# Kernel optimization log

Measured on AMD Instinct MI355X. Metric: run time of the kernel, lower is better.

Reference implementation:

```python
import jax, jax.numpy as jnp
import numpy as np

N_HEADS = 8
HEAD_DIM = 64  # d_model // n_heads = 512 // 8


def setup_inputs() -> dict:
    key = jax.random.key(0)
    kq, kk, kv, km = jax.random.split(key, 4)
    B, C, H, L, D = 8, 4, N_HEADS, 512, HEAD_DIM
    q = jax.random.normal(kq, (B * C, H, L, D), dtype=jnp.float32)
    k = jax.random.normal(kk, (B * C, H, D, L), dtype=jnp.float32)  # pre-transposed, matmul(q, k) directly
    v = jax.random.normal(kv, (B * C, H, L, D), dtype=jnp.float32)
    attn_mask = jax.random.randint(km, (B, L, L), 0, 2).astype(bool)  # True = masked out
    return {"q": q, "k": k, "v": v, "attn_mask": attn_mask}


def reference(q, k, v, attn_mask):
    # q: [B*C, H, L, D]; k: [B*C, H, D, L]; v: [B*C, H, L, D]; attn_mask: [B, L, L] bool
    scale = jnp.asarray(HEAD_DIM ** (-0.5), dtype=q.dtype)
    scores = jnp.einsum('ghld,ghdm->ghlm', q, k) * scale  # [B*C, H, L, L]
    if attn_mask is not None:
        B = attn_mask.shape[0]
        C = q.shape[0] // B
        H, L = scores.shape[1], scores.shape[2]
        scores = scores.reshape(B, C, H, L, L)
        mask = attn_mask[:, None, None, :, :]  # broadcast over channels and heads
        scores = jnp.where(mask, -jnp.inf, scores)
        scores = scores.reshape(B * C, H, L, L)
    attn_weights = jax.nn.softmax(scores, axis=-1)  # dropout p=0.0 -> identity (eval)
    output = jnp.einsum('ghlm,ghmd->ghld', attn_weights, v)  # [B*C, H, L, D]
    return output
```

## Files before the change

### kernel.cpp

```cpp
#include <hip/hip_runtime.h>


typedef __attribute__((ext_vector_type(8)))  short bf16x8;
typedef __attribute__((ext_vector_type(16))) float f32x16;

union Frag4 { uint4 x; unsigned u[4]; bf16x8 v; };

__device__ __forceinline__ unsigned pk_bf16(float a, float b){
    unsigned ua = __builtin_bit_cast(unsigned, a) + 0x8000u;
    unsigned ub = __builtin_bit_cast(unsigned, b) + 0x8000u;
    return __builtin_amdgcn_perm(ub, ua, 0x07060302u);
}

__device__ __forceinline__ float fast_exp2(float x){
#if __has_builtin(__builtin_amdgcn_exp2f)
    return __builtin_amdgcn_exp2f(x);
#else
    return exp2f(x);
#endif
}

#define L2E 1.44269504088896f

__global__ __launch_bounds__(256, 4)
void attn_fused(const float* __restrict__ qg, const float* __restrict__ kg,
                const float* __restrict__ vg, const int* __restrict__ mg,
                float* __restrict__ og)
{
    __shared__ uint4 sKt4[64*8];
    __shared__ uint4 sVt4[64*8];

    const int t    = threadIdx.x;
    const int lane = t & 63;
    const int wv   = t >> 6;
    const int col  = lane & 31;
    const int h    = lane >> 5;

    const int bi   = blockIdx.x;
    const int s    = bi >> 3;
    const int head = (bi & 7)*32 + (s >> 2);
    const int qt   = s & 3;
    const int b    = bi & 7;

    const float* qh = qg + (size_t)head*32768;
    const float* kh = kg + (size_t)head*32768;
    const float* vh = vg + (size_t)head*32768;
    const int*   mb = mg + (size_t)b*262144 + (size_t)qt*128*512;
    float*       oh = og + (size_t)head*32768;

    Frag4 qf[4];
    {
        const int qrow = qt*128 + wv*32 + col;
        const float* qr = qh + qrow*64 + h*8;
        #pragma unroll
        for (int kt=0; kt<4; ++kt){
            float4 x0 = *(const float4*)(qr + kt*16);
            float4 x1 = *(const float4*)(qr + kt*16 + 4);
            qf[kt].u[0] = pk_bf16(x0.x*0.125f, x0.y*0.125f);
            qf[kt].u[1] = pk_bf16(x0.z*0.125f, x0.w*0.125f);
            qf[kt].u[2] = pk_bf16(x1.x*0.125f, x1.y*0.125f);
            qf[kt].u[3] = pk_bf16(x1.z*0.125f, x1.w*0.125f);
        }
    }

    f32x16 o0, o1;
    #pragma unroll
    for (int i=0;i<16;++i){ o0[i]=0.f; o1[i]=0.f; }
    float lsum = 0.f;

    for (int kb=0; kb<8; ++kb){
        __syncthreads();
        #pragma unroll
        for (int gi=0; gi<2; ++gi){
            const int g = wv + gi*4;
            const float* kp = kh + (size_t)(g*8)*512 + kb*64 + lane;
            float kv[8];
            #pragma unroll
            for (int dd=0; dd<8; ++dd) kv[dd] = kp[(size_t)dd*512];
            Frag4 w;
            w.u[0]=pk_bf16(kv[0],kv[1]); w.u[1]=pk_bf16(kv[2],kv[3]);
            w.u[2]=pk_bf16(kv[4],kv[5]); w.u[3]=pk_bf16(kv[6],kv[7]);
            sKt4[lane*8 + (g ^ (lane&7))] = w.x;
        }
        #pragma unroll
        for (int gi=0; gi<2; ++gi){
            const int g = wv + gi*4;
            const float* vp = vh + (size_t)(kb*64 + g*8)*64 + lane;
            float vv[8];
            #pragma unroll
            for (int mm=0; mm<8; ++mm) vv[mm] = vp[(size_t)mm*64];
            Frag4 w;
            w.u[0]=pk_bf16(vv[0],vv[1]); w.u[1]=pk_bf16(vv[2],vv[3]);
            w.u[2]=pk_bf16(vv[4],vv[5]); w.u[3]=pk_bf16(vv[6],vv[7]);
            sVt4[lane*8 + (g ^ (lane&7))] = w.x;
        }
        __syncthreads();

        const int qrl = wv*32 + col;
        const int* mrow = mb + (size_t)qrl*512 + kb*64;
        #pragma unroll
        for (int mt=0; mt<2; ++mt){
            f32x16 sc;
            #pragma unroll
            for (int i=0;i<16;++i) sc[i]=0.f;
            #pragma unroll
            for (int kt=0; kt<4; ++kt){
                const int r = mt*32 + col;
                Frag4 a; a.x = sKt4[r*8 + ((kt*2+h) ^ (r&7))];
                sc = __builtin_amdgcn_mfma_f32_32x32x16_bf16(a.v, qf[kt].v, sc, 0, 0, 0);
            }
            float p[16];
            #pragma unroll
            for (int rg=0; rg<4; ++rg){
                int4 mm = *(const int4*)(mrow + mt*32 + rg*8 + h*4);
                float e0 = mm.x ? 0.f : fast_exp2(sc[4*rg+0]*L2E);
                float e1 = mm.y ? 0.f : fast_exp2(sc[4*rg+1]*L2E);
                float e2 = mm.z ? 0.f : fast_exp2(sc[4*rg+2]*L2E);
                float e3 = mm.w ? 0.f : fast_exp2(sc[4*rg+3]*L2E);
                p[4*rg+0]=e0; p[4*rg+1]=e1; p[4*rg+2]=e2; p[4*rg+3]=e3;
                lsum += (e0+e1)+(e2+e3);
            }
            unsigned pp[8];
            #pragma unroll
            for (int r2=0; r2<8; ++r2) pp[r2] = pk_bf16(p[2*r2], p[2*r2+1]);

            #pragma unroll
            for (int c=0; c<2; ++c){
                unsigned keep0 = h ? pp[4*c+2] : pp[4*c+0];
                unsigned keep1 = h ? pp[4*c+3] : pp[4*c+1];
                unsigned give0 = h ? pp[4*c+0] : pp[4*c+2];
                unsigned give1 = h ? pp[4*c+1] : pp[4*c+3];
                unsigned got0 = (unsigned)__shfl_xor((int)give0, 32, 64);
                unsigned got1 = (unsigned)__shfl_xor((int)give1, 32, 64);
                Frag4 pa;
                pa.u[0] = h ? got0  : keep0;
                pa.u[1] = h ? got1  : keep1;
                pa.u[2] = h ? keep0 : got0;
                pa.u[3] = h ? keep1 : got1;
                const int gm = mt*4 + c*2 + h;
                Frag4 b0; b0.x = sVt4[col*8      + (gm ^ (col&7))];
                o0 = __builtin_amdgcn_mfma_f32_32x32x16_bf16(pa.v, b0.v, o0, 0, 0, 0);
                Frag4 b1; b1.x = sVt4[(32+col)*8 + (gm ^ ((32+col)&7))];
                o1 = __builtin_amdgcn_mfma_f32_32x32x16_bf16(pa.v, b1.v, o1, 0, 0, 0);
            }
        }
    }

    lsum += __shfl_xor(lsum, 32, 64);
    const float inv = 1.0f / lsum;
    float* ob = oh + (size_t)(qt*128 + wv*32)*64;
    #pragma unroll
    for (int r=0; r<16; ++r){
        const int qq = (r&3) + 8*(r>>2) + 4*h;
        const float iv = __shfl(inv, qq, 64);
        ob[(size_t)qq*64 + col]      = o0[r]*iv;
        ob[(size_t)qq*64 + 32 + col] = o1[r]*iv;
    }
}

extern "C" void kernel_launch(void* const* d_in, const int* in_sizes, int n_in,
                              void* d_out, int out_size, void* d_ws, size_t ws_size,
                              hipStream_t stream) {
    (void)in_sizes; (void)n_in; (void)d_ws; (void)ws_size; (void)out_size;
    const float* q = (const float*)d_in[0];
    const float* k = (const float*)d_in[1];
    const float* v = (const float*)d_in[2];
    const int*   m = (const int*)d_in[3];
    attn_fused<<<dim3(1024), dim3(256), 0, stream>>>(q, k, v, m, (float*)d_out);
}
```

Measured before the change: 174.0 us.

## Double-buffer K/V shared tiles with register prefetch and fold log2e into Q scale

Introduces double-buffered shared memory for the K and V tiles. The next block's K/V global loads are issued into registers before the current block's MFMA and softmax work, and written to the other buffer afterwards, so only one barrier per iteration remains. Mask loads are hoisted ahead of the score MFMAs, and the log2(e) factor is folded into the Q prescale so no multiply is needed before exp2. This raises register and LDS pressure, which could hurt occupancy at the requested 4 blocks per CU.

After: 327.5 us. +88.2%, slower.

```diff
diff --git a/kernel.cpp b/kernel.cpp
--- a/kernel.cpp
+++ b/kernel.cpp
@@ -20,15 +20,15 @@
 #endif
 }
 
-#define L2E 1.44269504088896f
+#define SCL 0.1803368801111204f
 
 __global__ __launch_bounds__(256, 4)
 void attn_fused(const float* __restrict__ qg, const float* __restrict__ kg,
                 const float* __restrict__ vg, const int* __restrict__ mg,
                 float* __restrict__ og)
 {
-    __shared__ uint4 sKt4[64*8];
-    __shared__ uint4 sVt4[64*8];
+    __shared__ uint4 sKt4[2][64*8];
+    __shared__ uint4 sVt4[2][64*8];
 
     const int t    = threadIdx.x;
     const int lane = t & 63;
@@ -45,21 +45,20 @@
     const float* qh = qg + (size_t)head*32768;
     const float* kh = kg + (size_t)head*32768;
     const float* vh = vg + (size_t)head*32768;
-    const int*   mb = mg + (size_t)b*262144 + (size_t)qt*128*512;
+    const int*   mrow = mg + (size_t)b*262144 + (size_t)(qt*128 + wv*32 + col)*512;
     float*       oh = og + (size_t)head*32768;
 
     Frag4 qf[4];
     {
-        const int qrow = qt*128 + wv*32 + col;
-        const float* qr = qh + qrow*64 + h*8;
+        const float* qr = qh + (size_t)(qt*128 + wv*32 + col)*64 + h*8;
         #pragma unroll
         for (int kt=0; kt<4; ++kt){
             float4 x0 = *(const float4*)(qr + kt*16);
             float4 x1 = *(const float4*)(qr + kt*16 + 4);
-            qf[kt].u[0] = pk_bf16(x0.x*0.125f, x0.y*0.125f);
-            qf[kt].u[1] = pk_bf16(x0.z*0.125f, x0.w*0.125f);
-            qf[kt].u[2] = pk_bf16(x1.x*0.125f, x1.y*0.125f);
-            qf[kt].u[3] = pk_bf16(x1.z*0.125f, x1.w*0.125f);
+            qf[kt].u[0] = pk_bf16(x0.x*SCL, x0.y*SCL);
+            qf[kt].u[1] = pk_bf16(x0.z*SCL, x0.w*SCL);
+            qf[kt].u[2] = pk_bf16(x1.x*SCL, x1.y*SCL);
+            qf[kt].u[3] = pk_bf16(x1.z*SCL, x1.w*SCL);
         }
     }
 
@@ -68,62 +67,92 @@
     for (int i=0;i<16;++i){ o0[i]=0.f; o1[i]=0.f; }
     float lsum = 0.f;
 
-    for (int kb=0; kb<8; ++kb){
-        __syncthreads();
+    {
+        float nk[2][8], nv[2][8];
         #pragma unroll
         for (int gi=0; gi<2; ++gi){
             const int g = wv + gi*4;
-            const float* kp = kh + (size_t)(g*8)*512 + kb*64 + lane;
-            float kv[8];
-            #pragma unroll
-            for (int dd=0; dd<8; ++dd) kv[dd] = kp[(size_t)dd*512];
-            Frag4 w;
-            w.u[0]=pk_bf16(kv[0],kv[1]); w.u[1]=pk_bf16(kv[2],kv[3]);
-            w.u[2]=pk_bf16(kv[4],kv[5]); w.u[3]=pk_bf16(kv[6],kv[7]);
-            sKt4[lane*8 + (g ^ (lane&7))] = w.x;
+            const float* kp = kh + (size_t)(g*8)*512 + lane;
+            const float* vp = vh + (size_t)(g*8)*64 + lane;
+            #pragma unroll
+            for (int dd=0; dd<8; ++dd){
+                nk[gi][dd] = kp[(size_t)dd*512];
+                nv[gi][dd] = vp[(size_t)dd*64];
+            }
         }
         #pragma unroll
         for (int gi=0; gi<2; ++gi){
             const int g = wv + gi*4;
-            const float* vp = vh + (size_t)(kb*64 + g*8)*64 + lane;
-            float vv[8];
-            #pragma unroll
-            for (int mm=0; mm<8; ++mm) vv[mm] = vp[(size_t)mm*64];
-            Frag4 w;
-            w.u[0]=pk_bf16(vv[0],vv[1]); w.u[1]=pk_bf16(vv[2],vv[3]);
-            w.u[2]=pk_bf16(vv[4],vv[5]); w.u[3]=pk_bf16(vv[6],vv[7]);
-            sVt4[lane*8 + (g ^ (lane&7))] = w.x;
-        }
-        __syncthreads();
-
-        const int qrl = wv*32 + col;
-        const int* mrow = mb + (size_t)qrl*512 + kb*64;
-        #pragma unroll
-        for (int mt=0; mt<2; ++mt){
-            f32x16 sc;
-            #pragma unroll
-            for (int i=0;i<16;++i) sc[i]=0.f;
-            #pragma unroll
-            for (int kt=0; kt<4; ++kt){
-                const int r = mt*32 + col;
-                Frag4 a; a.x = sKt4[r*8 + ((kt*2+h) ^ (r&7))];
-                sc = __builtin_amdgcn_mfma_f32_32x32x16_bf16(a.v, qf[kt].v, sc, 0, 0, 0);
-            }
+            Frag4 wk, wvv;
+            #pragma unroll
+            for (int j=0; j<4; ++j){
+                wk.u[j]  = pk_bf16(nk[gi][2*j], nk[gi][2*j+1]);
+                wvv.u[j] = pk_bf16(nv[gi][2*j], nv[gi][2*j+1]);
+            }
+            sKt4[0][lane*8 + (g ^ (lane&7))] = wk.x;
+            sVt4[0][lane*8 + (g ^ (lane&7))] = wvv.x;
+        }
+    }
+    __syncthreads();
+
+    #pragma unroll
+    for (int kb=0; kb<8; ++kb){
+        const int cb = kb & 1;
+        const int nb = cb ^ 1;
+        const bool pre = (kb < 7);
+
+        float nk[2][8];
+        if (pre){
+            #pragma unroll
+            for (int gi=0; gi<2; ++gi){
+                const int g = wv + gi*4;
+                const float* kp = kh + (size_t)(g*8)*512 + (kb+1)*64 + lane;
+                #pragma unroll
+                for (int dd=0; dd<8; ++dd) nk[gi][dd] = kp[(size_t)dd*512];
+            }
+        }
+        int4 m0[4];
+        #pragma unroll
+        for (int rg=0; rg<4; ++rg)
+            m0[rg] = *(const int4*)(mrow + kb*64 + rg*8 + h*4);
+
+        f32x16 sc;
+        #pragma unroll
+        for (int i=0;i<16;++i) sc[i]=0.f;
+        #pragma unroll
+        for (int kt=0; kt<4; ++kt){
+            const int r = col;
+            Frag4 a; a.x = sKt4[cb][r*8 + ((kt*2+h) ^ (r&7))];
+            sc = __builtin_amdgcn_mfma_f32_32x32x16_bf16(a.v, qf[kt].v, sc, 0, 0, 0);
+        }
+        int4 m1[4];
+        #pragma unroll
+        for (int rg=0; rg<4; ++rg)
+            m1[rg] = *(const int4*)(mrow + kb*64 + 32 + rg*8 + h*4);
+        float nv[2][8];
+        if (pre){
+            #pragma unroll
+            for (int gi=0; gi<2; ++gi){
+                const int g = wv + gi*4;
+                const float* vp = vh + (size_t)((kb+1)*64 + g*8)*64 + lane;
+                #pragma unroll
+                for (int mm=0; mm<8; ++mm) nv[gi][mm] = vp[(size_t)mm*64];
+            }
+        }
+        {
             float p[16];
             #pragma unroll
             for (int rg=0; rg<4; ++rg){
-                int4 mm = *(const int4*)(mrow + mt*32 + rg*8 + h*4);
-                float e0 = mm.x ? 0.f : fast_exp2(sc[4*rg+0]*L2E);
-                float e1 = mm.y ? 0.f : fast_exp2(sc[4*rg+1]*L2E);
-                float e2 = mm.z ? 0.f : fast_exp2(sc[4*rg+2]*L2E);
-                float e3 = mm.w ? 0.f : fast_exp2(sc[4*rg+3]*L2E);
+                float e0 = m0[rg].x ? 0.f : fast_exp2(sc[4*rg+0]);
+                float e1 = m0[rg].y ? 0.f : fast_exp2(sc[4*rg+1]);
+                float e2 = m0[rg].z ? 0.f : fast_exp2(sc[4*rg+2]);
+                float e3 = m0[rg].w ? 0.f : fast_exp2(sc[4*rg+3]);
                 p[4*rg+0]=e0; p[4*rg+1]=e1; p[4*rg+2]=e2; p[4*rg+3]=e3;
                 lsum += (e0+e1)+(e2+e3);
             }
             unsigned pp[8];
             #pragma unroll
             for (int r2=0; r2<8; ++r2) pp[r2] = pk_bf16(p[2*r2], p[2*r2+1]);
-
             #pragma unroll
             for (int c=0; c<2; ++c){
                 unsigned keep0 = h ? pp[4*c+2] : pp[4*c+0];
@@ -137,12 +166,76 @@
                 pa.u[1] = h ? got1  : keep1;
                 pa.u[2] = h ? keep0 : got0;
                 pa.u[3] = h ? keep1 : got1;
-                const int gm = mt*4 + c*2 + h;
-                Frag4 b0; b0.x = sVt4[col*8      + (gm ^ (col&7))];
+                const int gm = c*2 + h;
+                Frag4 b0; b0.x = sVt4[cb][col*8      + (gm ^ (col&7))];
                 o0 = __builtin_amdgcn_mfma_f32_32x32x16_bf16(pa.v, b0.v, o0, 0, 0, 0);
-                Frag4 b1; b1.x = sVt4[(32+col)*8 + (gm ^ ((32+col)&7))];
+                Frag4 b1; b1.x = sVt4[cb][(32+col)*8 + (gm ^ ((32+col)&7))];
                 o1 = __builtin_amdgcn_mfma_f32_32x32x16_bf16(pa.v, b1.v, o1, 0, 0, 0);
             }
+        }
+        Frag4 wk[2];
+        if (pre){
+            #pragma unroll
+            for (int gi=0; gi<2; ++gi)
+                #pragma unroll
+                for (int j=0; j<4; ++j)
+                    wk[gi].u[j] = pk_bf16(nk[gi][2*j], nk[gi][2*j+1]);
+        }
+
+        #pragma unroll
+        for (int i=0;i<16;++i) sc[i]=0.f;
+        #pragma unroll
+        for (int kt=0; kt<4; ++kt){
+            const int r = 32 + col;
+            Frag4 a; a.x = sKt4[cb][r*8 + ((kt*2+h) ^ (r&7))];
+            sc = __builtin_amdgcn_mfma_f32_32x32x16_bf16(a.v, qf[kt].v, sc, 0, 0, 0);
+        }
+        {
+            float p[16];
+            #pragma unroll
+            for (int rg=0; rg<4; ++rg){
+                float e0 = m1[rg].x ? 0.f : fast_exp2(sc[4*rg+0]);
+                float e1 = m1[rg].y ? 0.f : fast_exp2(sc[4*rg+1]);
+                float e2 = m1[rg].z ? 0.f : fast_exp2(sc[4*rg+2]);
+                float e3 = m1[rg].w ? 0.f : fast_exp2(sc[4*rg+3]);
+                p[4*rg+0]=e0; p[4*rg+1]=e1; p[4*rg+2]=e2; p[4*rg+3]=e3;
+                lsum += (e0+e1)+(e2+e3);
+            }
+            unsigned pp[8];
+            #pragma unroll
+            for (int r2=0; r2<8; ++r2) pp[r2] = pk_bf16(p[2*r2], p[2*r2+1]);
+            #pragma unroll
+            for (int c=0; c<2; ++c){
+                unsigned keep0 = h ? pp[4*c+2] : pp[4*c+0];
+                unsigned keep1 = h ? pp[4*c+3] : pp[4*c+1];
+                unsigned give0 = h ? pp[4*c+0] : pp[4*c+2];
+                unsigned give1 = h ? pp[4*c+1] : pp[4*c+3];
+                unsigned got0 = (unsigned)__shfl_xor((int)give0, 32, 64);
+                unsigned got1 = (unsigned)__shfl_xor((int)give1, 32, 64);
+                Frag4 pa;
+                pa.u[0] = h ? got0  : keep0;
+                pa.u[1] = h ? got1  : keep1;
+                pa.u[2] = h ? keep0 : got0;
+                pa.u[3] = h ? keep1 : got1;
+                const int gm = 4 + c*2 + h;
+                Frag4 b0; b0.x = sVt4[cb][col*8      + (gm ^ (col&7))];
+                o0 = __builtin_amdgcn_mfma_f32_32x32x16_bf16(pa.v, b0.v, o0, 0, 0, 0);
+                Frag4 b1; b1.x = sVt4[cb][(32+col)*8 + (gm ^ ((32+col)&7))];
+                o1 = __builtin_amdgcn_mfma_f32_32x32x16_bf16(pa.v, b1.v, o1, 0, 0, 0);
+            }
+        }
+
+        if (pre){
+            #pragma unroll
+            for (int gi=0; gi<2; ++gi){
+                const int g = wv + gi*4;
+                Frag4 wvv;
+                #pragma unroll
+                for (int j=0; j<4; ++j) wvv.u[j] = pk_bf16(nv[gi][2*j], nv[gi][2*j+1]);
+                sKt4[nb][lane*8 + (g ^ (lane&7))] = wk[gi].x;
+                sVt4[nb][lane*8 + (g ^ (lane&7))] = wvv.x;
+            }
+            __syncthreads();
         }
     }
 
```
